# Kernel optimization log

Measured on AMD Instinct MI355X. Metric: run time of the kernel, lower is better.

The kernel has to match this reference:

```python
import jax, jax.numpy as jnp
import numpy as np

N, S, K, H, D = 8192, 16384, 16, 8, 512
E = N * K
HEAD_DIM = D // H


def setup_inputs() -> dict:
    key = jax.random.key(0)
    ks = jax.random.split(key, 12)
    x = jax.random.normal(ks[0], (N, D), jnp.float32)
    # every destination row gets K edges so softmax rows are never empty
    row_index = jnp.repeat(jnp.arange(N, dtype=jnp.int32), K)  # [E], sorted
    src_index = jax.random.randint(ks[1], (E,), 0, S, dtype=jnp.int32)
    att_bias = jax.random.normal(ks[2], (H, E), jnp.float32)
    dist = jax.random.uniform(ks[3], (E,), jnp.float32, minval=0.5, maxval=10.0)
    pos = jax.random.normal(ks[4], (N, 3), jnp.float32)
    src_pos = jax.random.normal(ks[5], (S, 3), jnp.float32)
    org_to_src = jax.random.randint(ks[6], (S,), 0, N, dtype=jnp.int32)
    scale = 1.0 / np.sqrt(D).astype(np.float32)
    Wq = jax.random.normal(ks[7], (D, D), jnp.float32) * scale
    bq = jax.random.normal(ks[8], (D,), jnp.float32) * 0.01
    Wk = jax.random.normal(ks[9], (D, D), jnp.float32) * scale
    bk = jax.random.normal(ks[10], (D,), jnp.float32) * 0.01
    return {"x": x, "row_index": row_index, "src_index": src_index,
            "att_bias": att_bias, "dist": dist, "pos": pos, "src_pos": src_pos,
            "org_to_src": org_to_src, "Wq": Wq, "bq": bq, "Wk": Wk, "bk": bk}


def reference(x, row_index, src_index, att_bias, dist, pos, src_pos, org_to_src,
              Wq, bq, Wk, bk):
    n, d_model = x.shape
    h, e = att_bias.shape
    hd = d_model // h
    # Projections -> [N, H, hd]; key gathered to the source list via org_to_src -> [S, H, hd]
    q = (x @ Wq + bq).reshape(n, h, hd)
    k_src = ((x @ Wk + bk).reshape(n, h, hd))[org_to_src]
    # Per-edge masked logits: (q/sqrt(hd)) . k + att_bias   (COO sparse attention)
    q_e = q[row_index]                       # [E, H, hd]
    k_e = k_src[src_index]                   # [E, H, hd]
    logits = jnp.einsum('ehd,ehd->eh', q_e, k_e) / np.sqrt(hd).astype(np.float32)
    logits = logits + att_bias.T             # [E, H]
    # Segment softmax over edges sharing a destination row
    m = jax.ops.segment_max(logits, row_index, num_segments=n)      # [N, H]
    p = jnp.exp(logits - m[row_index])
    z = jax.ops.segment_sum(p, row_index, num_segments=n)           # [N, H]
    att = p / z[row_index]                                          # [E, H]
    # Distance reweighting: 1/dist with dist==0 -> 0 weight
    safe = jnp.where(dist == 0, 1.0, dist)
    inv_d = jnp.where(dist == 0, 0.0, 1.0 / safe)
    att = att * inv_d[:, None]
    # dst_vec = att @ src_pos ; src_vec = (att @ 1) * pos   (both as segment sums)
    dst = jax.ops.segment_sum(att[:, :, None] * src_pos[src_index][:, None, :],
                              row_index, num_segments=n)            # [N, H, 3]
    asum = jax.ops.segment_sum(att, row_index, num_segments=n)      # [N, H]
    feat = dst - asum[:, :, None] * pos[:, None, :]                 # [N, H, 3]
    return feat.reshape(n, h * 3)
```

## Files before the change

kernel.cpp:

```cpp
#include <hip/hip_runtime.h>

#define N_ROWS 8192
#define D_MODEL 512
#define KT 512
#define NHEAD 8
#define KEDGE 16
#define NEDGE (N_ROWS * KEDGE)
#define BK 64

using f32x4  = __attribute__((ext_vector_type(4))) float;
using bf16x8 = __attribute__((ext_vector_type(8))) __bf16;
using u16x8  = __attribute__((ext_vector_type(8))) unsigned short;

__device__ __forceinline__ unsigned short bf16_rtne(float f) {
    unsigned u = __float_as_uint(f);
    u += 0x7FFFu + ((u >> 16) & 1u);
    return (unsigned short)(u >> 16);
}
__device__ __forceinline__ float from_bf16(unsigned short b) {
    return __uint_as_float(((unsigned)b) << 16);
}

#define GLOAD16(gp, lp) __builtin_amdgcn_global_load_lds( \
    (__attribute__((address_space(1))) void*)(void*)(gp), \
    (__attribute__((address_space(3))) void*)(lp), 16, 0, 0)

__global__ __launch_bounds__(256) void prep(const float* __restrict__ x,
                                            const float* __restrict__ Wq,
                                            const float* __restrict__ Wk,
                                            unsigned short* __restrict__ Xb,
                                            unsigned short* __restrict__ Bt) {
    if (blockIdx.x < 2048) {
        const int i = (blockIdx.x * 256 + threadIdx.x) * 8;
        const float4 a = *reinterpret_cast<const float4*>(x + i);
        const float4 b = *reinterpret_cast<const float4*>(x + i + 4);
        u16x8 o;
        o[0] = bf16_rtne(a.x); o[1] = bf16_rtne(a.y);
        o[2] = bf16_rtne(a.z); o[3] = bf16_rtne(a.w);
        o[4] = bf16_rtne(b.x); o[5] = bf16_rtne(b.y);
        o[6] = bf16_rtne(b.z); o[7] = bf16_rtne(b.w);
        *reinterpret_cast<u16x8*>(Xb + i) = o;
    } else {
        const int gid = (blockIdx.x - 2048) * 256 + threadIdx.x;
        const int j = gid >> 9;
        const int k = gid & 511;
        const float* W = (j < 512) ? Wq : Wk;
        Bt[(size_t)j * KT + k] = bf16_rtne(W[k * D_MODEL + (j & 511)]);
    }
}

__global__ __launch_bounds__(512) void gemm_qk(
    const unsigned short* __restrict__ Xb, const unsigned short* __restrict__ Bt,
    const float* __restrict__ bq, const float* __restrict__ bk,
    unsigned short* __restrict__ Qp, unsigned short* __restrict__ Kp)
{
    __shared__ __align__(16) unsigned short As[2][128 * BK];
    __shared__ __align__(16) unsigned short Bs[2][128 * BK];

    const int tid  = threadIdx.x;
    const int lane = tid & 63;
    const int wave = tid >> 6;
    const int wr   = wave >> 2;
    const int wc   = wave & 3;

    const int bid = blockIdx.x;
    const int xcd = bid & 7;
    const int j   = bid >> 3;
    const int rp  = xcd * 8 + (j >> 3);
    const int cp  = j & 7;
    const int row0 = rp * 128, col0 = cp * 128;

    f32x4 acc[4][2];
    #pragma unroll
    for (int m = 0; m < 4; ++m)
        #pragma unroll
        for (int n = 0; n < 2; ++n)
            acc[m][n] = (f32x4){0.f, 0.f, 0.f, 0.f};

    const int crow = tid >> 3;
    const int sc   = ((tid & 7) ^ (crow & 7)) * 8;

    const unsigned short* gA = Xb + (size_t)(row0 + crow) * D_MODEL + sc;
    const unsigned short* gB = Bt + (size_t)(col0 + crow) * KT     + sc;

    #define STAGE(b, kb) do { \
        GLOAD16(gA + (kb),                &As[b][tid * 8]); \
        GLOAD16(gA + (kb) + 64 * D_MODEL, &As[b][(tid + 512) * 8]); \
        GLOAD16(gB + (kb),                &Bs[b][tid * 8]); \
        GLOAD16(gB + (kb) + 64 * KT,      &Bs[b][(tid + 512) * 8]); \
    } while (0)

    STAGE(0, 0);
    __syncthreads();

    int buf = 0;
    for (int kt = 0; kt < KT / BK; ++kt) {
        if (kt < KT / BK - 1) STAGE(buf ^ 1, (kt + 1) * BK);
        #pragma unroll
        for (int kk = 0; kk < 2; ++kk) {
            const int kc = kk * 4 + (lane >> 4);
            bf16x8 afr[4], bfr[2];
            #pragma unroll
            for (int m = 0; m < 4; ++m) {
                const int r = wr * 64 + m * 16 + (lane & 15);
                afr[m] = __builtin_bit_cast(bf16x8, *reinterpret_cast<const u16x8*>(
                    &As[buf][r * BK + ((kc ^ (r & 7)) * 8)]));
            }
            #pragma unroll
            for (int n = 0; n < 2; ++n) {
                const int r = wc * 32 + n * 16 + (lane & 15);
                bfr[n] = __builtin_bit_cast(bf16x8, *reinterpret_cast<const u16x8*>(
                    &Bs[buf][r * BK + ((kc ^ (r & 7)) * 8)]));
            }
            #pragma unroll
            for (int m = 0; m < 4; ++m)
                #pragma unroll
                for (int n = 0; n < 2; ++n)
                    acc[m][n] = __builtin_amdgcn_mfma_f32_16x16x32_bf16(
                        afr[m], bfr[n], acc[m][n], 0, 0, 0);
        }
        __syncthreads();
        buf ^= 1;
    }
    #undef STAGE

    #pragma unroll
    for (int m = 0; m < 4; ++m) {
        const int row = row0 + wr * 64 + m * 16 + (lane >> 4) * 4;
        #pragma unroll
        for (int n = 0; n < 2; ++n) {
            const int c = col0 + wc * 32 + n * 16 + (lane & 15);
            const int cc = c & 511;
            unsigned short* plane = (c < 512) ? Qp : Kp;
            const float bias = (c < 512) ? bq[cc] : bk[cc];
            #pragma unroll
            for (int r = 0; r < 4; ++r)
                plane[(size_t)(row + r) * D_MODEL + cc] = bf16_rtne(acc[m][n][r] + bias);
        }
    }
}

__global__ __launch_bounds__(256) void edge_kernel(
    const unsigned short* __restrict__ Qp, const unsigned short* __restrict__ Kp,
    const int* __restrict__ src_index,
    const int* __restrict__ org_to_src,
    const float* __restrict__ att_bias,
    const float* __restrict__ dist,
    const float* __restrict__ pos,
    const float* __restrict__ src_pos,
    float* __restrict__ out)
{
    const int lane = threadIdx.x & 63;
    const int wave = threadIdx.x >> 6;
    const int n = blockIdx.x * 4 + wave;
    const int ll = lane & 31;
    const int half = lane >> 5;
    const int h = ll >> 2;
    const int o1 = h * 64 + (ll & 3) * 8;
    const int o2 = o1 + 32;

    int kne[8];
    float iv[8], spx[8], spy[8], spz[8], at[8];
    #pragma unroll
    for (int i = 0; i < 8; ++i) {
        const int ge = n * KEDGE + 2 * i + half;
        const int s = src_index[ge];
        kne[i] = org_to_src[s];
        const float d = dist[ge];
        iv[i] = (d == 0.f) ? 0.f : 1.f / d;
        spx[i] = src_pos[s * 3 + 0];
        spy[i] = src_pos[s * 3 + 1];
        spz[i] = src_pos[s * 3 + 2];
        at[i] = att_bias[(size_t)h * NEDGE + ge];
    }

    const u16x8 q1 = *reinterpret_cast<const u16x8*>(Qp + (size_t)n * D_MODEL + o1);
    const u16x8 q2 = *reinterpret_cast<const u16x8*>(Qp + (size_t)n * D_MODEL + o2);
    float qf1[8], qf2[8];
    #pragma unroll
    for (int i = 0; i < 8; ++i) { qf1[i] = from_bf16(q1[i]); qf2[i] = from_bf16(q2[i]); }

    float logit[8];
    #pragma unroll
    for (int i = 0; i < 8; ++i) {
        const unsigned short* kp = Kp + (size_t)kne[i] * D_MODEL;
        const u16x8 k1 = *reinterpret_cast<const u16x8*>(kp + o1);
        const u16x8 k2 = *reinterpret_cast<const u16x8*>(kp + o2);
        float p = 0.f;
        #pragma unroll
        for (int jj = 0; jj < 8; ++jj)
            p += qf1[jj] * from_bf16(k1[jj]) + qf2[jj] * from_bf16(k2[jj]);
        p += __shfl_xor(p, 1);
        p += __shfl_xor(p, 2);
        logit[i] = p * 0.125f + at[i];
    }

    float mx = logit[0];
    #pragma unroll
    for (int i = 1; i < 8; ++i) mx = fmaxf(mx, logit[i]);
    mx = fmaxf(mx, __shfl_xor(mx, 32));
    float pe[8];
    float z = 0.f;
    #pragma unroll
    for (int i = 0; i < 8; ++i) { pe[i] = __expf(logit[i] - mx); z += pe[i]; }
    z += __shfl_xor(z, 32);
    const float rz = 1.f / z;

    float d0 = 0.f, d1 = 0.f, d2 = 0.f, asum = 0.f;
    #pragma unroll
    for (int i = 0; i < 8; ++i) {
        const float w = pe[i] * rz * iv[i];
        d0 += w * spx[i]; d1 += w * spy[i]; d2 += w * spz[i];
        asum += w;
    }
    d0 += __shfl_xor(d0, 32);
    d1 += __shfl_xor(d1, 32);
    d2 += __shfl_xor(d2, 32);
    asum += __shfl_xor(asum, 32);

    const int c = ll & 3;
    if (half == 0 && c < 3) {
        const float dc = (c == 0) ? d0 : ((c == 1) ? d1 : d2);
        out[n * 24 + h * 3 + c] = dc - asum * pos[n * 3 + c];
    }
}

extern "C" void kernel_launch(void* const* d_in, const int* in_sizes, int n_in,
                              void* d_out, int out_size, void* d_ws, size_t ws_size,
                              hipStream_t stream) {
    const float* x          = (const float*)d_in[0];
    const int*   src_index  = (const int*)d_in[2];
    const float* att_bias   = (const float*)d_in[3];
    const float* dist       = (const float*)d_in[4];
    const float* pos        = (const float*)d_in[5];
    const float* src_pos    = (const float*)d_in[6];
    const int*   org_to_src = (const int*)d_in[7];
    const float* Wq         = (const float*)d_in[8];
    const float* bq         = (const float*)d_in[9];
    const float* Wk         = (const float*)d_in[10];
    const float* bk         = (const float*)d_in[11];
    float* out = (float*)d_out;

    char* ws = (char*)d_ws;
    unsigned short* Xb  = (unsigned short*)(ws);
    unsigned short* Bt  = (unsigned short*)(ws + ( 8u << 20));
    unsigned short* Qp  = (unsigned short*)(ws + ( 9u << 20));
    unsigned short* Kp  = (unsigned short*)(ws + (17u << 20));

    prep<<<dim3(4096), dim3(256), 0, stream>>>(x, Wq, Wk, Xb, Bt);
    gemm_qk<<<dim3(512), dim3(512), 0, stream>>>(Xb, Bt, bq, bk, Qp, Kp);
    edge_kernel<<<dim3(N_ROWS / 4), dim3(256), 0, stream>>>(
        Qp, Kp, src_index, org_to_src, att_bias, dist, pos, src_pos, out);
}
```

Before: 41.48 us.

## Split Q/K head dims into two planes and compute edge logits in two passes

The GEMM epilogue now writes Q and K as two half-width planes, one per 32-dim half of each head. The edge work becomes two kernels. The first computes partial dot products over the first half and stores them to a float buffer, and the second adds the second half and does the softmax and output. The intent is to shrink each pass's random-gather working set (4 MB per K plane) so it fits better in cache. The cost is an extra kernel launch, a partial-logit buffer round trip, and re-reading the indices.

```diff
diff --git a/kernel.cpp b/kernel.cpp
--- a/kernel.cpp
+++ b/kernel.cpp
@@ -7,6 +7,7 @@
 #define KEDGE 16
 #define NEDGE (N_ROWS * KEDGE)
 #define BK 64
+#define PLANE 256
 
 using f32x4  = __attribute__((ext_vector_type(4))) float;
 using bf16x8 = __attribute__((ext_vector_type(8))) __bf16;
@@ -52,7 +53,8 @@
 __global__ __launch_bounds__(512) void gemm_qk(
     const unsigned short* __restrict__ Xb, const unsigned short* __restrict__ Bt,
     const float* __restrict__ bq, const float* __restrict__ bk,
-    unsigned short* __restrict__ Qp, unsigned short* __restrict__ Kp)
+    unsigned short* __restrict__ QA, unsigned short* __restrict__ QB,
+    unsigned short* __restrict__ KA, unsigned short* __restrict__ KB)
 {
     __shared__ __align__(16) unsigned short As[2][128 * BK];
     __shared__ __align__(16) unsigned short Bs[2][128 * BK];
@@ -131,17 +133,58 @@
         for (int n = 0; n < 2; ++n) {
             const int c = col0 + wc * 32 + n * 16 + (lane & 15);
             const int cc = c & 511;
-            unsigned short* plane = (c < 512) ? Qp : Kp;
+            const int h = cc >> 6, din = cc & 63;
+            unsigned short* plane = (c < 512) ? ((din < 32) ? QA : QB)
+                                              : ((din < 32) ? KA : KB);
             const float bias = (c < 512) ? bq[cc] : bk[cc];
+            const int off = h * 32 + (din & 31);
             #pragma unroll
             for (int r = 0; r < 4; ++r)
-                plane[(size_t)(row + r) * D_MODEL + cc] = bf16_rtne(acc[m][n][r] + bias);
+                plane[(size_t)(row + r) * PLANE + off] = bf16_rtne(acc[m][n][r] + bias);
         }
     }
 }
 
-__global__ __launch_bounds__(256) void edge_kernel(
-    const unsigned short* __restrict__ Qp, const unsigned short* __restrict__ Kp,
+__global__ __launch_bounds__(256) void edge_a(
+    const unsigned short* __restrict__ QA, const unsigned short* __restrict__ KA,
+    const int* __restrict__ src_index, const int* __restrict__ org_to_src,
+    float* __restrict__ partial)
+{
+    const int lane = threadIdx.x & 63;
+    const int wave = threadIdx.x >> 6;
+    const int n = blockIdx.x * 4 + wave;
+    const int ll = lane & 31;
+    const int half = lane >> 5;
+    const int h = ll >> 2;
+    const int po = h * 32 + (ll & 3) * 8;
+
+    int kne[8];
+    #pragma unroll
+    for (int i = 0; i < 8; ++i)
+        kne[i] = org_to_src[src_index[n * KEDGE + 2 * i + half]];
+
+    const u16x8 qv = *reinterpret_cast<const u16x8*>(QA + (size_t)n * PLANE + po);
+    float qf[8];
+    #pragma unroll
+    for (int i = 0; i < 8; ++i) qf[i] = from_bf16(qv[i]);
+
+    #pragma unroll
+    for (int i = 0; i < 8; ++i) {
+        const u16x8 kv = *reinterpret_cast<const u16x8*>(
+            KA + (size_t)kne[i] * PLANE + po);
+        float p = 0.f;
+        #pragma unroll
+        for (int jj = 0; jj < 8; ++jj) p += qf[jj] * from_bf16(kv[jj]);
+        p += __shfl_xor(p, 1);
+        p += __shfl_xor(p, 2);
+        if ((ll & 3) == 0)
+            partial[(size_t)(n * KEDGE + 2 * i + half) * NHEAD + h] = p;
+    }
+}
+
+__global__ __launch_bounds__(256) void edge_b(
+    const unsigned short* __restrict__ QB, const unsigned short* __restrict__ KB,
+    const float* __restrict__ partial,
     const int* __restrict__ src_index,
     const int* __restrict__ org_to_src,
     const float* __restrict__ att_bias,
@@ -156,11 +199,10 @@
     const int ll = lane & 31;
     const int half = lane >> 5;
     const int h = ll >> 2;
-    const int o1 = h * 64 + (ll & 3) * 8;
-    const int o2 = o1 + 32;
+    const int po = h * 32 + (ll & 3) * 8;
 
     int kne[8];
-    float iv[8], spx[8], spy[8], spz[8], at[8];
+    float iv[8], spx[8], spy[8], spz[8], at[8], pp[8];
     #pragma unroll
     for (int i = 0; i < 8; ++i) {
         const int ge = n * KEDGE + 2 * i + half;
@@ -172,27 +214,25 @@
         spy[i] = src_pos[s * 3 + 1];
         spz[i] = src_pos[s * 3 + 2];
         at[i] = att_bias[(size_t)h * NEDGE + ge];
-    }
-
-    const u16x8 q1 = *reinterpret_cast<const u16x8*>(Qp + (size_t)n * D_MODEL + o1);
-    const u16x8 q2 = *reinterpret_cast<const u16x8*>(Qp + (size_t)n * D_MODEL + o2);
-    float qf1[8], qf2[8];
-    #pragma unroll
-    for (int i = 0; i < 8; ++i) { qf1[i] = from_bf16(q1[i]); qf2[i] = from_bf16(q2[i]); }
+        pp[i] = partial[(size_t)ge * NHEAD + h];
+    }
+
+    const u16x8 qv = *reinterpret_cast<const u16x8*>(QB + (size_t)n * PLANE + po);
+    float qf[8];
+    #pragma unroll
+    for (int i = 0; i < 8; ++i) qf[i] = from_bf16(qv[i]);
 
     float logit[8];
     #pragma unroll
     for (int i = 0; i < 8; ++i) {
-        const unsigned short* kp = Kp + (size_t)kne[i] * D_MODEL;
-        const u16x8 k1 = *reinterpret_cast<const u16x8*>(kp + o1);
-        const u16x8 k2 = *reinterpret_cast<const u16x8*>(kp + o2);
+        const u16x8 kv = *reinterpret_cast<const u16x8*>(
+            KB + (size_t)kne[i] * PLANE + po);
         float p = 0.f;
         #pragma unroll
-        for (int jj = 0; jj < 8; ++jj)
-            p += qf1[jj] * from_bf16(k1[jj]) + qf2[jj] * from_bf16(k2[jj]);
+        for (int jj = 0; jj < 8; ++jj) p += qf[jj] * from_bf16(kv[jj]);
         p += __shfl_xor(p, 1);
         p += __shfl_xor(p, 2);
-        logit[i] = p * 0.125f + at[i];
+        logit[i] = (p + pp[i]) * 0.125f + at[i];
     }
 
     float mx = logit[0];
@@ -244,11 +284,16 @@
     char* ws = (char*)d_ws;
     unsigned short* Xb  = (unsigned short*)(ws);
     unsigned short* Bt  = (unsigned short*)(ws + ( 8u << 20));
-    unsigned short* Qp  = (unsigned short*)(ws + ( 9u << 20));
-    unsigned short* Kp  = (unsigned short*)(ws + (17u << 20));
+    unsigned short* QA  = (unsigned short*)(ws + ( 9u << 20));
+    unsigned short* QB  = (unsigned short*)(ws + (13u << 20));
+    unsigned short* KA  = (unsigned short*)(ws + (17u << 20));
+    unsigned short* KB  = (unsigned short*)(ws + (21u << 20));
+    float*          Pt  = (float*)         (ws + (25u << 20));
 
     prep<<<dim3(4096), dim3(256), 0, stream>>>(x, Wq, Wk, Xb, Bt);
-    gemm_qk<<<dim3(512), dim3(512), 0, stream>>>(Xb, Bt, bq, bk, Qp, Kp);
-    edge_kernel<<<dim3(N_ROWS / 4), dim3(256), 0, stream>>>(
-        Qp, Kp, src_index, org_to_src, att_bias, dist, pos, src_pos, out);
-}
+    gemm_qk<<<dim3(512), dim3(512), 0, stream>>>(Xb, Bt, bq, bk, QA, QB, KA, KB);
+    edge_a<<<dim3(N_ROWS / 4), dim3(256), 0, stream>>>(
+        QA, KA, src_index, org_to_src, Pt);
+    edge_b<<<dim3(N_ROWS / 4), dim3(256), 0, stream>>>(
+        QB, KB, Pt, src_index, org_to_src, att_bias, dist, pos, src_pos, out);
+}
```

After: 44.86 us. 1.08x slower.
